# Kernel tuning notes

Measured on AMD Instinct MI355X. Metric: run time of the kernel, lower is better.

## Reference

```python
import jax, jax.numpy as jnp
import numpy as np

B, N, DIM, H = 2, 2048, 1024, 16
HD = DIM // H
SCALE = HD ** -0.5


def setup_inputs() -> dict:
    key = jax.random.key(0)
    ks = jax.random.split(key, 11)
    std = DIM ** -0.5
    inp = {
        'q': jax.random.normal(ks[0], (B, N, DIM), jnp.float32),
        'k': jax.random.normal(ks[1], (B, N, DIM), jnp.float32),
        'v': jax.random.normal(ks[2], (B, N, DIM), jnp.float32),
        # causal mask, broadcast over batch and heads; mask==0 -> masked out
        'mask': jnp.tril(jnp.ones((N, N), jnp.int32))[None, None],
        'Wq': jax.random.normal(ks[3], (DIM, DIM), jnp.float32) * std,
        'bq': jnp.zeros((DIM,), jnp.float32),
        'Wk': jax.random.normal(ks[4], (DIM, DIM), jnp.float32) * std,
        'bk': jnp.zeros((DIM,), jnp.float32),
        'Wv': jax.random.normal(ks[5], (DIM, DIM), jnp.float32) * std,
        'bv': jnp.zeros((DIM,), jnp.float32),
        'Wo': jax.random.normal(ks[6], (DIM, DIM), jnp.float32) * std,
        'bo': jnp.zeros((DIM,), jnp.float32),
    }
    return inp


def _split_heads(x):  # [b, n, dim] -> [b, h, n, c]
    b, n, _ = x.shape
    return x.reshape(b, n, H, HD).transpose(0, 2, 1, 3)


def reference(q, k, v, mask, Wq, bq, Wk, bk, Wv, bv, Wo, bo):
    qh = _split_heads(q @ Wq.T + bq)                      # [b,h,nq,c]
    kh = _split_heads(k @ Wk.T + bk)                      # [b,h,nk,c]
    vh = _split_heads(v @ Wv.T + bv)                      # [b,h,nk,c]
    attn = jnp.einsum('bhqc,bhkc->bhqk', qh, kh) * SCALE  # [b,h,nq,nk]
    attn = jnp.where(mask == 0, -jnp.inf, attn)
    attn = jax.nn.softmax(attn, axis=-1)
    out = jnp.einsum('bhqk,bhkc->bhqc', attn, vh)          # [b,h,nq,c]
    b, h, n, c = out.shape
    out = out.transpose(0, 2, 1, 3).reshape(b, n, h * c)   # [b,nq,dim]
    return out @ Wo.T + bo
```

## Files before the change

### kernel.cpp

```cpp
#include <hip/hip_runtime.h>

#define NN 2048
#define DIMD 1024
#define HH 16
#define HDD 64
#define SC2 0.1803368801111244f

typedef __attribute__((ext_vector_type(8))) short bf16x8;
typedef __attribute__((ext_vector_type(4))) float f32x4;
typedef unsigned short ushort_t;
typedef unsigned int uint_t;

#if __has_builtin(__builtin_amdgcn_exp2f)
#define EXP2(x) __builtin_amdgcn_exp2f(x)
#else
#define EXP2(x) exp2f(x)
#endif

__device__ __forceinline__ ushort_t f2bf(float f) {
    union { float f; uint_t u; } v; v.f = f;
    uint_t u = v.u;
    return (ushort_t)((u + 0x7FFFu + ((u >> 16) & 1u)) >> 16);
}
__device__ __forceinline__ ushort_t f2bf_trunc(float f) {
    union { float f; uint_t u; } v; v.f = f;
    return (ushort_t)(v.u >> 16);
}
__device__ __forceinline__ void gl_lds16(const ushort_t* g, ushort_t* l) {
    __builtin_amdgcn_global_load_lds(
        (const __attribute__((address_space(1))) void*)g,
        (__attribute__((address_space(3))) void*)l, 16, 0, 0);
}

__global__ __launch_bounds__(256) void convert_k(
    const float* __restrict__ q, const float* __restrict__ k, const float* __restrict__ v,
    const float* __restrict__ wq, const float* __restrict__ wk,
    const float* __restrict__ wv, const float* __restrict__ wo,
    ushort_t* __restrict__ Abf, ushort_t* __restrict__ Wbf) {
    size_t gid = (size_t)blockIdx.x * 256 + threadIdx.x;
    size_t e = gid * 8;
    const float* src; ushort_t* dst;
    float sc = 1.f;
    if (e < 12582912) {
        int i = (int)(e >> 22);
        src = (i == 0 ? q : (i == 1 ? k : v)) + (e & 4194303);
        dst = Abf + e;
    } else {
        size_t e2 = e - 12582912;
        int i = (int)(e2 >> 20);
        src = (i == 0 ? wq : (i == 1 ? wk : (i == 2 ? wv : wo))) + (e2 & 1048575);
        dst = Wbf + e2;
        if (i == 0) sc = SC2;
    }
    float4 x = ((const float4*)src)[0], y = ((const float4*)src)[1];
    union { uint4 u; ushort_t s[8]; } pk;
    pk.s[0] = f2bf(x.x * sc); pk.s[1] = f2bf(x.y * sc); pk.s[2] = f2bf(x.z * sc); pk.s[3] = f2bf(x.w * sc);
    pk.s[4] = f2bf(y.x * sc); pk.s[5] = f2bf(y.y * sc); pk.s[6] = f2bf(y.z * sc); pk.s[7] = f2bf(y.w * sc);
    *(uint4*)dst = pk.u;
}

template<int MODE>
__global__ __launch_bounds__(256) void gemm_k(
    const ushort_t* __restrict__ Abase, const ushort_t* __restrict__ Wbase,
    const float* __restrict__ b0p, const float* __restrict__ b1p, const float* __restrict__ b2p,
    ushort_t* __restrict__ d0, ushort_t* __restrict__ d1, ushort_t* __restrict__ d2,
    float* __restrict__ fout) {
    const int K = 1024;
    __shared__ ushort_t As[128 * 32];
    __shared__ ushort_t Bs[128 * 32];
    int z = (MODE == 0) ? blockIdx.z : 0;
    const ushort_t* A = Abase + (size_t)z * 4096 * 1024;
    const ushort_t* W = Wbase + (size_t)z * 1024 * 1024;
    const float* bias = (MODE == 0) ? (z == 0 ? b0p : (z == 1 ? b1p : b2p)) : b0p;
    int tid = threadIdx.x;
    int m0 = blockIdx.x * 128, n0 = blockIdx.y * 128;
    int lane = tid & 63, wave = tid >> 6;
    int quad = lane >> 4, l15 = lane & 15;
    int wm = (wave >> 1) * 64, wn = (wave & 1) * 64;

    f32x4 acc[4][4];
    for (int i = 0; i < 4; i++)
        for (int j = 0; j < 4; j++)
            acc[i][j] = (f32x4){0.f, 0.f, 0.f, 0.f};

    for (int k0 = 0; k0 < K; k0 += 32) {
        __syncthreads();
        for (int c = 0; c < 2; c++) {
            int lin = tid + c * 256;
            int r = lin >> 2, cg = lin & 3;
            gl_lds16(A + (size_t)(m0 + r) * K + k0 + cg * 8, &As[lin * 8]);
            gl_lds16(W + (size_t)(n0 + r) * K + k0 + cg * 8, &Bs[lin * 8]);
        }
        __syncthreads();
        bf16x8 a[4], b[4];
        for (int mt = 0; mt < 4; mt++)
            a[mt] = *(const bf16x8*)&As[(wm + mt * 16 + l15) * 32 + quad * 8];
        for (int nt = 0; nt < 4; nt++)
            b[nt] = *(const bf16x8*)&Bs[(wn + nt * 16 + l15) * 32 + quad * 8];
        for (int mt = 0; mt < 4; mt++)
            for (int nt = 0; nt < 4; nt++)
                acc[mt][nt] = __builtin_amdgcn_mfma_f32_16x16x32_bf16(a[mt], b[nt], acc[mt][nt], 0, 0, 0);
    }
    for (int nt = 0; nt < 4; nt++) {
        int n = n0 + wn + nt * 16 + l15;
        float bv = bias[n];
        if (MODE == 0 && z == 0) bv *= SC2;
        for (int mt = 0; mt < 4; mt++)
            for (int r = 0; r < 4; r++) {
                int m = m0 + wm + mt * 16 + quad * 4 + r;
                float val = acc[mt][nt][r] + bv;
                if (MODE == 0) {
                    int b = m >> 11, ns = m & 2047;
                    int h = n >> 6, c = n & 63;
                    if (z == 2)
                        d2[(((size_t)(b * HH + h)) * HDD + c) * NN + ns] = f2bf(val);
                    else {
                        ushort_t* dst = (z == 0) ? d0 : d1;
                        dst[(((size_t)(b * HH + h)) * NN + ns) * HDD + c] = f2bf(val);
                    }
                } else {
                    fout[(size_t)m * DIMD + n] = val;
                }
            }
    }
}

__global__ __launch_bounds__(256, 4) void attn3(const ushort_t* __restrict__ Qh,
                                                const ushort_t* __restrict__ Kh,
                                                const ushort_t* __restrict__ VtG,
                                                ushort_t* __restrict__ aout) {
    __shared__ ushort_t Ks[64 * 72];
    __shared__ ushort_t Vs[64 * 72];
    __shared__ ushort_t Ps[4][16 * 72];
    int tid = threadIdx.x, lane = tid & 63, w = tid >> 6;
    int quad = lane >> 4, l15 = lane & 15;
    int bh = blockIdx.y;
    int x = blockIdx.x;
    int qb = (x & 1) ? (31 - (x >> 1)) : (x >> 1);
    const ushort_t* Qp = Qh + (size_t)bh * NN * HDD;
    const ushort_t* Kp = Kh + (size_t)bh * NN * HDD;
    const ushort_t* Vp = VtG + (size_t)bh * HDD * NN;
    int row_lo = qb * 64 + w * 16;

    bf16x8 aq[2];
    for (int kc = 0; kc < 2; kc++)
        aq[kc] = *(const bf16x8*)&Qp[(size_t)(row_lo + l15) * HDD + kc * 32 + quad * 8];

    f32x4 o[4];
    float l_acc[4];
    for (int ct = 0; ct < 4; ct++) o[ct] = (f32x4){0.f, 0.f, 0.f, 0.f};
    for (int r = 0; r < 4; r++) l_acc[r] = 0.f;

    for (int kb = 0; kb <= qb; kb++) {
        __syncthreads();
        for (int p = 0; p < 2; p++) {
            int lin = tid + p * 256;
            int r = lin >> 3, cg = lin & 7;
            *(uint4*)&Ks[r * 72 + cg * 8] = *(const uint4*)&Kp[(size_t)(kb * 64 + r) * HDD + cg * 8];
            *(uint4*)&Vs[r * 72 + cg * 8] = *(const uint4*)&Vp[(size_t)r * NN + kb * 64 + cg * 8];
        }
        __syncthreads();

        f32x4 s[4];
        for (int nt = 0; nt < 4; nt++) {
            bf16x8 b0 = *(const bf16x8*)&Ks[(nt * 16 + l15) * 72 + quad * 8];
            bf16x8 b1 = *(const bf16x8*)&Ks[(nt * 16 + l15) * 72 + 32 + quad * 8];
            f32x4 zz = (f32x4){0.f, 0.f, 0.f, 0.f};
            zz = __builtin_amdgcn_mfma_f32_16x16x32_bf16(aq[0], b0, zz, 0, 0, 0);
            s[nt] = __builtin_amdgcn_mfma_f32_16x16x32_bf16(aq[1], b1, zz, 0, 0, 0);
        }
        if (kb == qb) {
            for (int nt = 0; nt < 4; nt++)
                for (int r = 0; r < 4; r++) {
                    int kv = kb * 64 + nt * 16 + l15;
                    int qq = row_lo + quad * 4 + r;
                    float p = (kv <= qq) ? EXP2(s[nt][r]) : 0.f;
                    s[nt][r] = p;
                    l_acc[r] += p;
                }
        } else {
            for (int nt = 0; nt < 4; nt++)
                for (int r = 0; r < 4; r++) {
                    float p = EXP2(s[nt][r]);
                    s[nt][r] = p;
                    l_acc[r] += p;
                }
        }
        for (int nt = 0; nt < 4; nt++)
            for (int r = 0; r < 4; r++)
                Ps[w][(quad * 4 + r) * 72 + nt * 16 + l15] = f2bf_trunc(s[nt][r]);
        bf16x8 ap0 = *(const bf16x8*)&Ps[w][l15 * 72 + quad * 8];
        bf16x8 ap1 = *(const bf16x8*)&Ps[w][l15 * 72 + 32 + quad * 8];
        for (int ct = 0; ct < 4; ct++) {
            bf16x8 bv0 = *(const bf16x8*)&Vs[(ct * 16 + l15) * 72 + quad * 8];
            bf16x8 bv1 = *(const bf16x8*)&Vs[(ct * 16 + l15) * 72 + 32 + quad * 8];
            o[ct] = __builtin_amdgcn_mfma_f32_16x16x32_bf16(ap0, bv0, o[ct], 0, 0, 0);
            o[ct] = __builtin_amdgcn_mfma_f32_16x16x32_bf16(ap1, bv1, o[ct], 0, 0, 0);
        }
    }
    float rl[4];
    for (int r = 0; r < 4; r++) {
        float t = l_acc[r];
        for (int d = 1; d < 16; d <<= 1) t += __shfl_xor(t, d);
        rl[r] = 1.f / t;
    }
    int b = bh >> 4, h = bh & 15;
    for (int ct = 0; ct < 4; ct++)
        for (int r = 0; r < 4; r++) {
            int qq = row_lo + quad * 4 + r;
            int c = ct * 16 + l15;
            aout[((size_t)(b * NN + qq)) * DIMD + h * HDD + c] = f2bf(o[ct][r] * rl[r]);
        }
}

extern "C" void kernel_launch(void* const* d_in, const int* in_sizes, int n_in,
                              void* d_out, int out_size, void* d_ws, size_t ws_size,
                              hipStream_t stream) {
    const float* q  = (const float*)d_in[0];
    const float* k  = (const float*)d_in[1];
    const float* v  = (const float*)d_in[2];
    const float* Wq = (const float*)d_in[4];
    const float* bq = (const float*)d_in[5];
    const float* Wk = (const float*)d_in[6];
    const float* bk = (const float*)d_in[7];
    const float* Wv = (const float*)d_in[8];
    const float* bv = (const float*)d_in[9];
    const float* Wo = (const float*)d_in[10];
    const float* bo = (const float*)d_in[11];
    float* out = (float*)d_out;

    char* ws = (char*)d_ws;
    ushort_t* Abf  = (ushort_t*)(ws);
    ushort_t* Wbf  = (ushort_t*)(ws + (24ull << 20));
    ushort_t* Qh   = (ushort_t*)(ws + (32ull << 20));
    ushort_t* Kh   = (ushort_t*)(ws + (40ull << 20));
    ushort_t* VtG  = (ushort_t*)(ws + (48ull << 20));
    ushort_t* AObf = (ushort_t*)(ws + (56ull << 20));

    hipLaunchKernelGGL(convert_k, dim3(8192), dim3(256), 0, stream,
                       q, k, v, Wq, Wk, Wv, Wo, Abf, Wbf);
    hipLaunchKernelGGL((gemm_k<0>), dim3(32, 8, 3), dim3(256), 0, stream,
                       Abf, Wbf, bq, bk, bv, Qh, Kh, VtG, (float*)nullptr);
    hipLaunchKernelGGL(attn3, dim3(32, 32), dim3(256), 0, stream, Qh, Kh, VtG, AObf);
    hipLaunchKernelGGL((gemm_k<1>), dim3(32, 8, 1), dim3(256), 0, stream,
                       AObf, Wbf + 3ull * 1024 * 1024, bo, nullptr, nullptr,
                       nullptr, nullptr, nullptr, out);
}
```

Before: 263.3 us.

## Double-buffer LDS tiles in GEMM and attention with async global-to-LDS loads

The GEMM and the attention kernel now keep two LDS buffers each. The next K/V or A/W tile is issued through global_load_lds while the current tile feeds MFMA, so each iteration needs one barrier instead of two. The attention kernel also drops its padded register-staged copies and uses an XOR swizzle on K, V and P tiles to avoid LDS bank conflicts. In exchange it doubles LDS use, which may lower occupancy, and it switches the exp2 builtin to exp2f, which may cost extra instructions.

```diff
diff --git a/kernel.cpp b/kernel.cpp
--- a/kernel.cpp
+++ b/kernel.cpp
@@ -10,12 +10,6 @@
 typedef __attribute__((ext_vector_type(4))) float f32x4;
 typedef unsigned short ushort_t;
 typedef unsigned int uint_t;
-
-#if __has_builtin(__builtin_amdgcn_exp2f)
-#define EXP2(x) __builtin_amdgcn_exp2f(x)
-#else
-#define EXP2(x) exp2f(x)
-#endif
 
 __device__ __forceinline__ ushort_t f2bf(float f) {
     union { float f; uint_t u; } v; v.f = f;
@@ -66,8 +60,8 @@
     ushort_t* __restrict__ d0, ushort_t* __restrict__ d1, ushort_t* __restrict__ d2,
     float* __restrict__ fout) {
     const int K = 1024;
-    __shared__ ushort_t As[128 * 32];
-    __shared__ ushort_t Bs[128 * 32];
+    __shared__ ushort_t As[2][128 * 32];
+    __shared__ ushort_t Bs[2][128 * 32];
     int z = (MODE == 0) ? blockIdx.z : 0;
     const ushort_t* A = Abase + (size_t)z * 4096 * 1024;
     const ushort_t* W = Wbase + (size_t)z * 1024 * 1024;
@@ -83,20 +77,29 @@
         for (int j = 0; j < 4; j++)
             acc[i][j] = (f32x4){0.f, 0.f, 0.f, 0.f};
 
-    for (int k0 = 0; k0 < K; k0 += 32) {
+    int r0 = tid >> 2, cg0 = tid & 3;
+    int r1 = (tid + 256) >> 2, cg1 = tid & 3;
+
+    gl_lds16(A + (size_t)(m0 + r0) * K + cg0 * 8, &As[0][(0 * 256 + wave * 64) * 8]);
+    gl_lds16(W + (size_t)(n0 + r0) * K + cg0 * 8, &Bs[0][(0 * 256 + wave * 64) * 8]);
+    gl_lds16(A + (size_t)(m0 + r1) * K + cg1 * 8, &As[0][(1 * 256 + wave * 64) * 8]);
+    gl_lds16(W + (size_t)(n0 + r1) * K + cg1 * 8, &Bs[0][(1 * 256 + wave * 64) * 8]);
+
+    for (int it = 0; it < 32; it++) {
+        int cur = it & 1;
         __syncthreads();
-        for (int c = 0; c < 2; c++) {
-            int lin = tid + c * 256;
-            int r = lin >> 2, cg = lin & 3;
-            gl_lds16(A + (size_t)(m0 + r) * K + k0 + cg * 8, &As[lin * 8]);
-            gl_lds16(W + (size_t)(n0 + r) * K + k0 + cg * 8, &Bs[lin * 8]);
-        }
-        __syncthreads();
+        if (it < 31) {
+            int k0 = (it + 1) * 32, nb = 1 - cur;
+            gl_lds16(A + (size_t)(m0 + r0) * K + k0 + cg0 * 8, &As[nb][(0 * 256 + wave * 64) * 8]);
+            gl_lds16(W + (size_t)(n0 + r0) * K + k0 + cg0 * 8, &Bs[nb][(0 * 256 + wave * 64) * 8]);
+            gl_lds16(A + (size_t)(m0 + r1) * K + k0 + cg1 * 8, &As[nb][(1 * 256 + wave * 64) * 8]);
+            gl_lds16(W + (size_t)(n0 + r1) * K + k0 + cg1 * 8, &Bs[nb][(1 * 256 + wave * 64) * 8]);
+        }
         bf16x8 a[4], b[4];
         for (int mt = 0; mt < 4; mt++)
-            a[mt] = *(const bf16x8*)&As[(wm + mt * 16 + l15) * 32 + quad * 8];
+            a[mt] = *(const bf16x8*)&As[cur][(wm + mt * 16 + l15) * 32 + quad * 8];
         for (int nt = 0; nt < 4; nt++)
-            b[nt] = *(const bf16x8*)&Bs[(wn + nt * 16 + l15) * 32 + quad * 8];
+            b[nt] = *(const bf16x8*)&Bs[cur][(wn + nt * 16 + l15) * 32 + quad * 8];
         for (int mt = 0; mt < 4; mt++)
             for (int nt = 0; nt < 4; nt++)
                 acc[mt][nt] = __builtin_amdgcn_mfma_f32_16x16x32_bf16(a[mt], b[nt], acc[mt][nt], 0, 0, 0);
@@ -125,13 +128,13 @@
     }
 }
 
-__global__ __launch_bounds__(256, 4) void attn3(const ushort_t* __restrict__ Qh,
+__global__ __launch_bounds__(256, 4) void attn4(const ushort_t* __restrict__ Qh,
                                                 const ushort_t* __restrict__ Kh,
                                                 const ushort_t* __restrict__ VtG,
                                                 ushort_t* __restrict__ aout) {
-    __shared__ ushort_t Ks[64 * 72];
-    __shared__ ushort_t Vs[64 * 72];
-    __shared__ ushort_t Ps[4][16 * 72];
+    __shared__ ushort_t Kb[2][64 * 64];
+    __shared__ ushort_t Vb[2][64 * 64];
+    __shared__ ushort_t Ps[4][16 * 64];
     int tid = threadIdx.x, lane = tid & 63, w = tid >> 6;
     int quad = lane >> 4, l15 = lane & 15;
     int bh = blockIdx.y;
@@ -151,20 +154,37 @@
     for (int ct = 0; ct < 4; ct++) o[ct] = (f32x4){0.f, 0.f, 0.f, 0.f};
     for (int r = 0; r < 4; r++) l_acc[r] = 0.f;
 
+    int sr0 = tid >> 3, scg0 = tid & 7;
+    int sr1 = (tid + 256) >> 3, scg1 = tid & 7;
+    int ssc0 = scg0 ^ (sr0 & 7);
+    int ssc1 = scg1 ^ (sr1 & 7);
+
+    int key = l15 & 7;
+    int c0 = (quad ^ key) * 8;
+    int c1 = ((4 + quad) ^ key) * 8;
+
+    {
+        gl_lds16(Kp + sr0 * 64 + ssc0 * 8, &Kb[0][(0 * 256 + w * 64) * 8]);
+        gl_lds16(Kp + sr1 * 64 + ssc1 * 8, &Kb[0][(1 * 256 + w * 64) * 8]);
+        gl_lds16(Vp + (size_t)sr0 * NN + ssc0 * 8, &Vb[0][(0 * 256 + w * 64) * 8]);
+        gl_lds16(Vp + (size_t)sr1 * NN + ssc1 * 8, &Vb[0][(1 * 256 + w * 64) * 8]);
+    }
+
     for (int kb = 0; kb <= qb; kb++) {
+        int cur = kb & 1;
         __syncthreads();
-        for (int p = 0; p < 2; p++) {
-            int lin = tid + p * 256;
-            int r = lin >> 3, cg = lin & 7;
-            *(uint4*)&Ks[r * 72 + cg * 8] = *(const uint4*)&Kp[(size_t)(kb * 64 + r) * HDD + cg * 8];
-            *(uint4*)&Vs[r * 72 + cg * 8] = *(const uint4*)&Vp[(size_t)r * NN + kb * 64 + cg * 8];
-        }
-        __syncthreads();
+        if (kb < qb) {
+            int nb = 1 - cur, kn = kb + 1;
+            gl_lds16(Kp + (size_t)(kn * 64 + sr0) * 64 + ssc0 * 8, &Kb[nb][(0 * 256 + w * 64) * 8]);
+            gl_lds16(Kp + (size_t)(kn * 64 + sr1) * 64 + ssc1 * 8, &Kb[nb][(1 * 256 + w * 64) * 8]);
+            gl_lds16(Vp + (size_t)sr0 * NN + kn * 64 + ssc0 * 8, &Vb[nb][(0 * 256 + w * 64) * 8]);
+            gl_lds16(Vp + (size_t)sr1 * NN + kn * 64 + ssc1 * 8, &Vb[nb][(1 * 256 + w * 64) * 8]);
+        }
 
         f32x4 s[4];
         for (int nt = 0; nt < 4; nt++) {
-            bf16x8 b0 = *(const bf16x8*)&Ks[(nt * 16 + l15) * 72 + quad * 8];
-            bf16x8 b1 = *(const bf16x8*)&Ks[(nt * 16 + l15) * 72 + 32 + quad * 8];
+            bf16x8 b0 = *(const bf16x8*)&Kb[cur][(nt * 16 + l15) * 64 + c0];
+            bf16x8 b1 = *(const bf16x8*)&Kb[cur][(nt * 16 + l15) * 64 + c1];
             f32x4 zz = (f32x4){0.f, 0.f, 0.f, 0.f};
             zz = __builtin_amdgcn_mfma_f32_16x16x32_bf16(aq[0], b0, zz, 0, 0, 0);
             s[nt] = __builtin_amdgcn_mfma_f32_16x16x32_bf16(aq[1], b1, zz, 0, 0, 0);
@@ -174,26 +194,29 @@
                 for (int r = 0; r < 4; r++) {
                     int kv = kb * 64 + nt * 16 + l15;
                     int qq = row_lo + quad * 4 + r;
-                    float p = (kv <= qq) ? EXP2(s[nt][r]) : 0.f;
+                    float p = (kv <= qq) ? exp2f(s[nt][r]) : 0.f;
                     s[nt][r] = p;
                     l_acc[r] += p;
                 }
         } else {
             for (int nt = 0; nt < 4; nt++)
                 for (int r = 0; r < 4; r++) {
-                    float p = EXP2(s[nt][r]);
+                    float p = exp2f(s[nt][r]);
                     s[nt][r] = p;
                     l_acc[r] += p;
                 }
         }
         for (int nt = 0; nt < 4; nt++)
-            for (int r = 0; r < 4; r++)
-                Ps[w][(quad * 4 + r) * 72 + nt * 16 + l15] = f2bf_trunc(s[nt][r]);
-        bf16x8 ap0 = *(const bf16x8*)&Ps[w][l15 * 72 + quad * 8];
-        bf16x8 ap1 = *(const bf16x8*)&Ps[w][l15 * 72 + 32 + quad * 8];
+            for (int r = 0; r < 4; r++) {
+                int qr = quad * 4 + r;
+                int cc = (nt * 2 + (l15 >> 3)) ^ (qr & 7);
+                Ps[w][qr * 64 + cc * 8 + (l15 & 7)] = f2bf_trunc(s[nt][r]);
+            }
+        bf16x8 ap0 = *(const bf16x8*)&Ps[w][l15 * 64 + c0];
+        bf16x8 ap1 = *(const bf16x8*)&Ps[w][l15 * 64 + c1];
         for (int ct = 0; ct < 4; ct++) {
-            bf16x8 bv0 = *(const bf16x8*)&Vs[(ct * 16 + l15) * 72 + quad * 8];
-            bf16x8 bv1 = *(const bf16x8*)&Vs[(ct * 16 + l15) * 72 + 32 + quad * 8];
+            bf16x8 bv0 = *(const bf16x8*)&Vb[cur][(ct * 16 + l15) * 64 + c0];
+            bf16x8 bv1 = *(const bf16x8*)&Vb[cur][(ct * 16 + l15) * 64 + c1];
             o[ct] = __builtin_amdgcn_mfma_f32_16x16x32_bf16(ap0, bv0, o[ct], 0, 0, 0);
             o[ct] = __builtin_amdgcn_mfma_f32_16x16x32_bf16(ap1, bv1, o[ct], 0, 0, 0);
         }
@@ -241,7 +264,7 @@
                        q, k, v, Wq, Wk, Wv, Wo, Abf, Wbf);
     hipLaunchKernelGGL((gemm_k<0>), dim3(32, 8, 3), dim3(256), 0, stream,
                        Abf, Wbf, bq, bk, bv, Qh, Kh, VtG, (float*)nullptr);
-    hipLaunchKernelGGL(attn3, dim3(32, 32), dim3(256), 0, stream, Qh, Kh, VtG, AObf);
+    hipLaunchKernelGGL(attn4, dim3(32, 32), dim3(256), 0, stream, Qh, Kh, VtG, AObf);
     hipLaunchKernelGGL((gemm_k<1>), dim3(32, 8, 1), dim3(256), 0, stream,
                        AObf, Wbf + 3ull * 1024 * 1024, bo, nullptr, nullptr,
                        nullptr, nullptr, nullptr, out);
```

Result: no change. 258.6 us (-1.8%).
